# Kernel optimization log

Measured on AMD Instinct MI355X. Metric: run time of the kernel, lower is better.

Reference implementation:

```python
import jax, jax.numpy as jnp
import numpy as np

B, S, D, H, L = 64, 2048, 768, 768, 2


def setup_inputs() -> dict:
    key = jax.random.key(0)
    ks = jax.random.split(key, 6)
    s = 1.0 / np.sqrt(H)
    x = jax.random.normal(ks[0], (B, S, D), dtype=jnp.float32)
    participants = jax.random.randint(ks[1], (S,), 0, 2, dtype=jnp.int32)
    W_ih = jax.random.uniform(ks[2], (L, 4 * H, D), jnp.float32, -s, s)
    W_hh = jax.random.uniform(ks[3], (L, 4 * H, H), jnp.float32, -s, s)
    b_ih = jax.random.uniform(ks[4], (L, 4 * H), jnp.float32, -s, s)
    b_hh = jax.random.uniform(ks[5], (L, 4 * H), jnp.float32, -s, s)
    return {"x": x, "W_ih": W_ih, "W_hh": W_hh, "b_ih": b_ih, "b_hh": b_hh,
            "participants": participants}


def _lstm_cell(inp, c, Wih, bi, bh):
    # PyTorch LSTMCell math. NOTE: the original module always passes h0 = zeros,
    # so the W_hh @ h0 term is identically zero and is omitted (same math,
    # and grad w.r.t. W_hh is zero, matching torch).
    gates = inp @ Wih.T + (bi + bh)  # [B, 4H]
    i, f, g, o = jnp.split(gates, 4, axis=-1)  # torch gate order: i, f, g, o
    i = jax.nn.sigmoid(i)
    f = jax.nn.sigmoid(f)
    g = jnp.tanh(g)
    o = jax.nn.sigmoid(o)
    c1 = f * c + i * g
    h1 = o * jnp.tanh(c1)
    return h1, c1


def reference(x, W_ih, W_hh, b_ih, b_hh, participants):
    # x: [B, S, D]; participants: [S] int speaker ids.
    # Quirks reproduced faithfully:
    #  - hidden state fed into every cell is always zeros (only cell state carries)
    #  - speaker change resets ONLY layer 0's cell state (last_speaker is updated
    #    inside the layer loop, so deeper layers never see the mismatch)
    #  - torch.clamp result is discarded in the original -> no clipping here
    Bx, Sx, _ = x.shape
    Hs = W_hh.shape[2]
    Ls = W_ih.shape[0]
    # reset[t] = True iff speaker changed; t=0 always resets (last_speaker=None)
    reset = jnp.concatenate([jnp.array([True]),
                             participants[1:] != participants[:-1]])  # [S] bool
    xs = (jnp.transpose(x, (1, 0, 2)), reset)  # ([S,B,D], [S])

    c_init = jnp.zeros((Ls, Bx, Hs), dtype=x.dtype)
    h_init = jnp.zeros((Ls, Bx, Hs), dtype=x.dtype)

    def step(carry, xt):
        hs, cs = carry  # each [L, B, H]
        inp_t, r = xt
        new_h, new_c = [], []
        h = None
        for l in range(Ls):
            c_in = cs[l]
            if l == 0:
                c_in = jnp.where(r, jnp.zeros_like(c_in), c_in)
            inp = inp_t if l == 0 else h
            h, c = _lstm_cell(inp, c_in, W_ih[l], b_ih[l], b_hh[l])
            new_h.append(h)
            new_c.append(c)
        return (jnp.stack(new_h), jnp.stack(new_c)), h

    (h_fin, c_fin), outputs = jax.lax.scan(step, (h_init, c_init), xs)
    # outputs: [S, B, H] (matches torch layout outputs[sequence, :, :H])
    return outputs, h_fin, c_fin
```

## Files before the change

### kernel.cpp

```cpp
#include <hip/hip_runtime.h>


typedef __attribute__((ext_vector_type(8))) short short8;
typedef __attribute__((ext_vector_type(4))) float floatx4;

#define B_ 64
#define S_ 2048
#define K_ 768
#define NG_ 3072

__device__ __forceinline__ unsigned short f2bf(float f) {
  unsigned int u = __builtin_bit_cast(unsigned int, f);
  u += 0x7fffu + ((u >> 16) & 1u);
  return (unsigned short)(u >> 16);
}

__device__ __forceinline__ float fsig(float x) {
  return __builtin_amdgcn_rcpf(1.f + __expf(-x));
}
__device__ __forceinline__ float mytanh(float x) {
  float e = __expf(-2.f * fabsf(x));
  float r = (1.f - e) * __builtin_amdgcn_rcpf(1.f + e);
  return __builtin_copysignf(r, x);
}

__device__ __forceinline__ void async16(const void* g, void* l) {
  __builtin_amdgcn_global_load_lds((__attribute__((address_space(1))) void*)g,
                                   (__attribute__((address_space(3))) void*)l,
                                   16, 0, 0);
}


__global__ __launch_bounds__(256) void prep_w(const float4* __restrict__ w4,
                                              ushort4* __restrict__ o4) {
  int idx = blockIdx.x * 256 + threadIdx.x;
  float4 v = w4[idx];
  ushort4 r;
  r.x = f2bf(v.x); r.y = f2bf(v.y); r.z = f2bf(v.z); r.w = f2bf(v.w);
  o4[idx] = r;
}

__global__ __launch_bounds__(256) void prep_small(const float* __restrict__ bih,
                                                  const float* __restrict__ bhh,
                                                  const int* __restrict__ parts,
                                                  float* __restrict__ bias,
                                                  int* __restrict__ rst) {
  int tid = blockIdx.x * 256 + threadIdx.x;
  if (tid < 2 * NG_) {
    bias[tid] = bih[tid] + bhh[tid];
  } else {
    int t = tid - 2 * NG_;
    rst[t] = (t == 0) ? 1 : ((parts[t] != parts[t - 1]) ? 1 : 0);
  }
}

__global__ __launch_bounds__(256) void cast_x(const float4* __restrict__ x4,
                                              ushort4* __restrict__ a4, int t0) {
  int idx = blockIdx.x * 256 + threadIdx.x;
  int m = idx / 192;
  int j = idx - m * 192;
  int b = m & 63, dt = m >> 6;
  float4 v = x4[((size_t)b * S_ + t0 + dt) * 192 + j];
  ushort4 r;
  r.x = f2bf(v.x); r.y = f2bf(v.y); r.z = f2bf(v.z); r.w = f2bf(v.w);
  a4[(size_t)m * 192 + j] = r;
}

__global__ __launch_bounds__(256) void gemm_bt(const unsigned short* __restrict__ A,
                                               const unsigned short* __restrict__ Bw,
                                               const float* __restrict__ bias,
                                               float* __restrict__ C) {
  __shared__ __align__(16) unsigned short At[128 * 64];
  __shared__ __align__(16) unsigned short Bt[128 * 64];
  const int tid = threadIdx.x;
  const int lane = tid & 63;
  const int wave = tid >> 6;
  const int wm = wave & 1, wn = wave >> 1;
  const int bm = blockIdx.x, bn = blockIdx.y;

  floatx4 acc[4][4] = {};

  const int rl = tid >> 3;
  const int cp = tid & 7;
  const size_t arow0 = (size_t)bm * 128;
  const size_t brow0 = (size_t)bn * 128;
  const int l15 = lane & 15, q = lane >> 4, sw = lane & 7;

  for (int kt = 0; kt < K_ / 64; ++kt) {
    const int k0 = kt * 64;
#pragma unroll
    for (int j = 0; j < 4; ++j) {
      int r = j * 32 + rl;
      int cl = cp ^ (r & 7);
      async16(A + (arow0 + r) * K_ + k0 + cl * 8, &At[r * 64 + cp * 8]);
      async16(Bw + (brow0 + r) * K_ + k0 + cl * 8, &Bt[r * 64 + cp * 8]);
    }
    __syncthreads();
#pragma unroll
    for (int ks = 0; ks < 2; ++ks) {
      short8 af[4], bf[4];
#pragma unroll
      for (int i = 0; i < 4; ++i) {
        int am = wm * 64 + i * 16 + l15;
        int bn_ = wn * 64 + i * 16 + l15;
        af[i] = *(const short8*)&At[am * 64 + ((ks * 4 + q) ^ sw) * 8];
        bf[i] = *(const short8*)&Bt[bn_ * 64 + ((ks * 4 + q) ^ sw) * 8];
      }
#pragma unroll
      for (int mi = 0; mi < 4; ++mi)
#pragma unroll
        for (int ni = 0; ni < 4; ++ni)
          acc[mi][ni] = __builtin_amdgcn_mfma_f32_16x16x32_bf16(
              af[mi], bf[ni], acc[mi][ni], 0, 0, 0);
    }
    __syncthreads();
  }

  const bool isg = (bn >= 12) && (bn < 18);
  if (isg) {
#pragma unroll
    for (int ni = 0; ni < 4; ++ni) {
      int col = bn * 128 + wn * 64 + ni * 16 + l15;
      float bs = bias[col];
#pragma unroll
      for (int mi = 0; mi < 4; ++mi) {
        int row = bm * 128 + wm * 64 + mi * 16 + q * 4;
#pragma unroll
        for (int r = 0; r < 4; ++r)
          C[(size_t)(row + r) * NG_ + col] = mytanh(acc[mi][ni][r] + bs);
      }
    }
  } else {
#pragma unroll
    for (int ni = 0; ni < 4; ++ni) {
      int col = bn * 128 + wn * 64 + ni * 16 + l15;
      float bs = bias[col];
#pragma unroll
      for (int mi = 0; mi < 4; ++mi) {
        int row = bm * 128 + wm * 64 + mi * 16 + q * 4;
#pragma unroll
        for (int r = 0; r < 4; ++r)
          C[(size_t)(row + r) * NG_ + col] = fsig(acc[mi][ni][r] + bs);
      }
    }
  }
}

template <int LAYER>
__global__ __launch_bounds__(64) void scan_kernel(
    const float* __restrict__ G, int Tc, int t0, const int* __restrict__ rst,
    float* __restrict__ carry, unsigned short* __restrict__ h0c,
    float* __restrict__ out, float* __restrict__ hfin, float* __restrict__ cfin) {
  const int b = blockIdx.x / 12;
  const int h = (blockIdx.x % 12) * 64 + threadIdx.x;
  const int ci = b * K_ + h;
  float c = (t0 == 0) ? 0.f : carry[ci];

  float va[8], vf[8], vg[8], vo[8];
#pragma unroll
  for (int d = 0; d < 8; ++d) {
    size_t base = ((size_t)(d * B_ + b)) * NG_ + h;
    va[d] = G[base];
    vf[d] = G[base + 768];
    vg[d] = G[base + 1536];
    vo[d] = G[base + 2304];
  }
  for (int dt0 = 0; dt0 < Tc; dt0 += 8) {
#pragma unroll
    for (int u = 0; u < 8; ++u) {
      const int dt = dt0 + u;
      const int t = t0 + dt;
      float av = va[u], fv = vf[u], gv = vg[u], ov = vo[u];
      int pre = dt + 8;
      if (pre < Tc) {
        size_t base = ((size_t)(pre * B_ + b)) * NG_ + h;
        va[u] = G[base];
        vf[u] = G[base + 768];
        vg[u] = G[base + 1536];
        vo[u] = G[base + 2304];
      }
      if (LAYER == 0) {
        if (rst[t]) c = 0.f;
      }
      c = fv * c + av * gv;
      float hv = ov * mytanh(c);
      if (LAYER == 0)
        h0c[((size_t)(dt * B_ + b)) * K_ + h] = f2bf(hv);
      else
        out[((size_t)(t * B_ + b)) * K_ + h] = hv;
      if (t == S_ - 1) { hfin[ci] = hv; cfin[ci] = c; }
    }
  }
  carry[ci] = c;
}


extern "C" void kernel_launch(void* const* d_in, const int* in_sizes, int n_in,
                              void* d_out, int out_size, void* d_ws, size_t ws_size,
                              hipStream_t stream) {
  const float* x = (const float*)d_in[0];
  const float* Wih = (const float*)d_in[1];
  const float* bih = (const float*)d_in[3];
  const float* bhh = (const float*)d_in[4];
  const int* parts = (const int*)d_in[5];

  char* ws = (char*)d_ws;
  unsigned short* Wbf = (unsigned short*)(ws);
  float* bias = (float*)(ws + 9437184);
  int* reset = (int*)(ws + 9461760);
  float* carry = (float*)(ws + 9469952);
  const size_t fixed_end = 9863168;

  float* out0 = (float*)d_out;
  float* hfin = out0 + 100663296LL;
  float* cfin = hfin + 98304;

  int chunk = 8;
  const int cand[5] = {128, 64, 32, 16, 8};
  for (int i = 0; i < 5; ++i) {
    size_t need = fixed_end + (size_t)cand[i] * 983040ull;
    if (need <= ws_size) { chunk = cand[i]; break; }
  }
  size_t off = fixed_end;
  unsigned short* Ah = (unsigned short*)(ws + off); off += (size_t)chunk * 98304;
  unsigned short* h0c = (unsigned short*)(ws + off); off += (size_t)chunk * 98304;
  float* Gc = (float*)(ws + off);

  prep_w<<<4608, 256, 0, stream>>>((const float4*)Wih, (ushort4*)Wbf);
  prep_small<<<32, 256, 0, stream>>>(bih, bhh, parts, bias, reset);

  const unsigned short* W0 = Wbf;
  const unsigned short* W1 = Wbf + (size_t)NG_ * K_;
  const int nch = S_ / chunk;
  const dim3 gg(chunk * B_ / 128, NG_ / 128);

  for (int ci = 0; ci < nch; ++ci) {
    const int t0 = ci * chunk;
    cast_x<<<chunk * 48, 256, 0, stream>>>((const float4*)x, (ushort4*)Ah, t0);
    gemm_bt<<<gg, 256, 0, stream>>>(Ah, W0, bias, Gc);
    scan_kernel<0><<<768, 64, 0, stream>>>(Gc, chunk, t0, reset, carry, h0c,
                                           nullptr, hfin, cfin);
    gemm_bt<<<gg, 256, 0, stream>>>(h0c, W1, bias + NG_, Gc);
    scan_kernel<1><<<768, 64, 0, stream>>>(Gc, chunk, t0, nullptr, carry + 49152,
                                           nullptr, out0, hfin + 49152,
                                           cfin + 49152);
  }
}
```

Before: 4.290 ms.

## Rewrite gate GEMM with 256x256 tiles and double-buffered async LDS pipeline

The gate GEMM moves from 128x128 tiles with 256 threads to 256x256 tiles with 512 threads. K-slabs are double-buffered in LDS, and the global-to-LDS loads for the next slab are split into quarter stages that interleave with MFMA work, synchronised through vmcnt waits and barriers. MFMA sections get raised wave priority. This targets load latency exposed by the old single-buffered loop and increases operand reuse, at the cost of more LDS (64KB), more accumulator registers, and fewer blocks per grid for small chunks.

```diff
diff --git a/kernel.cpp b/kernel.cpp
--- a/kernel.cpp
+++ b/kernel.cpp
@@ -8,6 +8,7 @@
 #define S_ 2048
 #define K_ 768
 #define NG_ 3072
+#define NT_ 12
 
 __device__ __forceinline__ unsigned short f2bf(float f) {
   unsigned int u = __builtin_bit_cast(unsigned int, f);
@@ -66,81 +67,120 @@
   a4[(size_t)m * 192 + j] = r;
 }
 
-__global__ __launch_bounds__(256) void gemm_bt(const unsigned short* __restrict__ A,
+__global__ __launch_bounds__(512) void gemm_bt(const unsigned short* __restrict__ A,
                                                const unsigned short* __restrict__ Bw,
                                                const float* __restrict__ bias,
                                                float* __restrict__ C) {
-  __shared__ __align__(16) unsigned short At[128 * 64];
-  __shared__ __align__(16) unsigned short Bt[128 * 64];
+  __shared__ __align__(16) unsigned short At[2][256 * 64];
+  __shared__ __align__(16) unsigned short Bt[2][256 * 64];
   const int tid = threadIdx.x;
   const int lane = tid & 63;
   const int wave = tid >> 6;
-  const int wm = wave & 1, wn = wave >> 1;
+  const int wm = wave >> 2;
+  const int wn = wave & 3;
   const int bm = blockIdx.x, bn = blockIdx.y;
-
-  floatx4 acc[4][4] = {};
-
-  const int rl = tid >> 3;
-  const int cp = tid & 7;
-  const size_t arow0 = (size_t)bm * 128;
-  const size_t brow0 = (size_t)bn * 128;
-  const int l15 = lane & 15, q = lane >> 4, sw = lane & 7;
-
-  for (int kt = 0; kt < K_ / 64; ++kt) {
-    const int k0 = kt * 64;
-#pragma unroll
-    for (int j = 0; j < 4; ++j) {
-      int r = j * 32 + rl;
-      int cl = cp ^ (r & 7);
-      async16(A + (arow0 + r) * K_ + k0 + cl * 8, &At[r * 64 + cp * 8]);
-      async16(Bw + (brow0 + r) * K_ + k0 + cl * 8, &Bt[r * 64 + cp * 8]);
-    }
-    __syncthreads();
-#pragma unroll
-    for (int ks = 0; ks < 2; ++ks) {
-      short8 af[4], bf[4];
-#pragma unroll
-      for (int i = 0; i < 4; ++i) {
-        int am = wm * 64 + i * 16 + l15;
-        int bn_ = wn * 64 + i * 16 + l15;
-        af[i] = *(const short8*)&At[am * 64 + ((ks * 4 + q) ^ sw) * 8];
-        bf[i] = *(const short8*)&Bt[bn_ * 64 + ((ks * 4 + q) ^ sw) * 8];
-      }
-#pragma unroll
-      for (int mi = 0; mi < 4; ++mi)
-#pragma unroll
-        for (int ni = 0; ni < 4; ++ni)
-          acc[mi][ni] = __builtin_amdgcn_mfma_f32_16x16x32_bf16(
-              af[mi], bf[ni], acc[mi][ni], 0, 0, 0);
-    }
-    __syncthreads();
-  }
-
-  const bool isg = (bn >= 12) && (bn < 18);
+  const int l15 = lane & 15, q = lane >> 4;
+
+  floatx4 acc[8][4] = {};
+
+  const int ci0 = tid, ci1 = 512 + tid;
+  const int r0 = ci0 >> 3, cp0 = ci0 & 7;
+  const int r1 = ci1 >> 3, cp1 = ci1 & 7;
+  const int cl0 = cp0 ^ (r0 & 7), cl1 = cp1 ^ (r1 & 7);
+
+  auto stage = [&](int t, int h) {
+    const int buf = t & 1;
+    const int k0 = t * 64;
+    const int half = h & 1;
+    if (h < 2) {
+      const unsigned short* src = A + ((size_t)(bm * 256 + half * 128)) * K_ + k0;
+      unsigned short* dst = &At[buf][half * 128 * 64];
+      async16(src + (size_t)r0 * K_ + cl0 * 8, dst + ci0 * 8);
+      async16(src + (size_t)r1 * K_ + cl1 * 8, dst + ci1 * 8);
+    } else {
+      const unsigned short* src = Bw + ((size_t)(bn * 256 + half * 128)) * K_ + k0;
+      unsigned short* dst = &Bt[buf][half * 128 * 64];
+      async16(src + (size_t)r0 * K_ + cl0 * 8, dst + ci0 * 8);
+      async16(src + (size_t)r1 * K_ + cl1 * 8, dst + ci1 * 8);
+    }
+  };
+
+  stage(0, 0); stage(0, 1); stage(0, 2); stage(0, 3); stage(1, 0);
+
+  short8 bfr[4][2];
+
+  for (int t = 0; t < NT_; ++t) {
+    const int buf = t & 1;
+#pragma unroll
+    for (int qd = 0; qd < 4; ++qd) {
+      if (qd == 0) {
+        if (t == NT_ - 1)
+          asm volatile("s_waitcnt vmcnt(0)" ::: "memory");
+        else
+          asm volatile("s_waitcnt vmcnt(2)" ::: "memory");
+        __builtin_amdgcn_s_barrier();
+#pragma unroll
+        for (int nf = 0; nf < 4; ++nf) {
+          int row = wn * 64 + nf * 16 + l15;
+#pragma unroll
+          for (int ks = 0; ks < 2; ++ks)
+            bfr[nf][ks] =
+                *(const short8*)&Bt[buf][row * 64 + (((ks * 4 + q) ^ (row & 7)) * 8)];
+        }
+      }
+      short8 afr[2][2];
+#pragma unroll
+      for (int mi = 0; mi < 2; ++mi) {
+        int row = (qd * 2 + mi) * 32 + wm * 16 + l15;
+#pragma unroll
+        for (int ks = 0; ks < 2; ++ks)
+          afr[mi][ks] =
+              *(const short8*)&At[buf][row * 64 + (((ks * 4 + q) ^ (row & 7)) * 8)];
+      }
+      if (qd == 0) { if (t + 1 < NT_) stage(t + 1, 1); }
+      else if (qd == 1) { if (t + 1 < NT_) stage(t + 1, 2); }
+      else if (qd == 2) { if (t + 1 < NT_) stage(t + 1, 3); }
+      else { if (t + 2 < NT_) stage(t + 2, 0); }
+      __builtin_amdgcn_s_barrier();
+      __builtin_amdgcn_s_setprio(1);
+#pragma unroll
+      for (int mi = 0; mi < 2; ++mi)
+#pragma unroll
+        for (int nf = 0; nf < 4; ++nf)
+#pragma unroll
+          for (int ks = 0; ks < 2; ++ks)
+            acc[qd * 2 + mi][nf] = __builtin_amdgcn_mfma_f32_16x16x32_bf16(
+                afr[mi][ks], bfr[nf][ks], acc[qd * 2 + mi][nf], 0, 0, 0);
+      __builtin_amdgcn_s_setprio(0);
+      __builtin_amdgcn_s_barrier();
+    }
+  }
+
+  const bool isg = (bn / 3) == 2;
   if (isg) {
 #pragma unroll
-    for (int ni = 0; ni < 4; ++ni) {
-      int col = bn * 128 + wn * 64 + ni * 16 + l15;
+    for (int nf = 0; nf < 4; ++nf) {
+      int col = bn * 256 + wn * 64 + nf * 16 + l15;
       float bs = bias[col];
 #pragma unroll
-      for (int mi = 0; mi < 4; ++mi) {
-        int row = bm * 128 + wm * 64 + mi * 16 + q * 4;
+      for (int mf = 0; mf < 8; ++mf) {
+        int row = bm * 256 + mf * 32 + wm * 16 + q * 4;
 #pragma unroll
         for (int r = 0; r < 4; ++r)
-          C[(size_t)(row + r) * NG_ + col] = mytanh(acc[mi][ni][r] + bs);
+          C[(size_t)(row + r) * NG_ + col] = mytanh(acc[mf][nf][r] + bs);
       }
     }
   } else {
 #pragma unroll
-    for (int ni = 0; ni < 4; ++ni) {
-      int col = bn * 128 + wn * 64 + ni * 16 + l15;
+    for (int nf = 0; nf < 4; ++nf) {
+      int col = bn * 256 + wn * 64 + nf * 16 + l15;
       float bs = bias[col];
 #pragma unroll
-      for (int mi = 0; mi < 4; ++mi) {
-        int row = bm * 128 + wm * 64 + mi * 16 + q * 4;
+      for (int mf = 0; mf < 8; ++mf) {
+        int row = bm * 256 + mf * 32 + wm * 16 + q * 4;
 #pragma unroll
         for (int r = 0; r < 4; ++r)
-          C[(size_t)(row + r) * NG_ + col] = fsig(acc[mi][ni][r] + bs);
+          C[(size_t)(row + r) * NG_ + col] = fsig(acc[mf][nf][r] + bs);
       }
     }
   }
@@ -232,15 +272,15 @@
   const unsigned short* W0 = Wbf;
   const unsigned short* W1 = Wbf + (size_t)NG_ * K_;
   const int nch = S_ / chunk;
-  const dim3 gg(chunk * B_ / 128, NG_ / 128);
+  const dim3 gg(chunk * B_ / 256, NG_ / 256);
 
   for (int ci = 0; ci < nch; ++ci) {
     const int t0 = ci * chunk;
     cast_x<<<chunk * 48, 256, 0, stream>>>((const float4*)x, (ushort4*)Ah, t0);
-    gemm_bt<<<gg, 256, 0, stream>>>(Ah, W0, bias, Gc);
+    gemm_bt<<<gg, 512, 0, stream>>>(Ah, W0, bias, Gc);
     scan_kernel<0><<<768, 64, 0, stream>>>(Gc, chunk, t0, reset, carry, h0c,
                                            nullptr, hfin, cfin);
-    gemm_bt<<<gg, 256, 0, stream>>>(h0c, W1, bias + NG_, Gc);
+    gemm_bt<<<gg, 512, 0, stream>>>(h0c, W1, bias + NG_, Gc);
     scan_kernel<1><<<768, 64, 0, stream>>>(Gc, chunk, t0, nullptr, carry + 49152,
                                            nullptr, out0, hfin + 49152,
                                            cfin + 49152);
```

New measurement: 4.524 ms. 5.5% more time.
